# Kernel tuning notes

Measured on AMD Instinct MI355X. Metric: run time of the kernel, lower is better.

## Reference

```python
import jax, jax.numpy as jnp
import numpy as np

LN_EPS = 1e-12
NEG_INF = -1e9


def setup_inputs() -> dict:
    key = jax.random.key(0)
    ks = jax.random.split(key, 4)
    B, S, H = 8, 2048, 1024
    inputs = jax.random.normal(ks[0], (B, S, H), dtype=jnp.float32)
    masks = jnp.ones((B, S), dtype=jnp.int32)
    scale = 1.0 / np.sqrt(H)
    Wq = jax.random.normal(ks[1], (H, H), dtype=jnp.float32) * scale
    bq = jnp.zeros((H,), dtype=jnp.float32)
    Wk = jax.random.normal(ks[2], (H, H), dtype=jnp.float32) * scale
    bk = jnp.zeros((H,), dtype=jnp.float32)
    ln_gamma = jnp.ones((H,), dtype=jnp.float32)
    ln_beta = jnp.zeros((H,), dtype=jnp.float32)
    return {"inputs": inputs, "masks": masks, "Wq": Wq, "bq": bq,
            "Wk": Wk, "bk": bk, "ln_gamma": ln_gamma, "ln_beta": ln_beta}


def _layernorm(x, gamma, beta):
    mu = jnp.mean(x, axis=-1, keepdims=True)
    var = jnp.mean(jnp.square(x - mu), axis=-1, keepdims=True)
    return (x - mu) * jax.lax.rsqrt(var + LN_EPS) * gamma + beta


def reference(inputs, masks, Wq, bq, Wk, bk, ln_gamma, ln_beta):
    # inputs: [B,S,H]; masks: [B,S] (1 = keep key position)
    H = inputs.shape[-1]
    query = inputs @ Wq + bq                      # [B,S,H]
    key_ = inputs @ Wk + bk                       # [B,S,H]
    scores = jnp.einsum('bqh,bkh->bqk', query, key_) * (1.0 / jnp.sqrt(jnp.float32(H)))
    # logits_mask: invalid key positions get large negative logit
    scores = jnp.where(masks[:, None, :] != 0, scores, NEG_INF)
    probs = jax.nn.softmax(scores, axis=-1)       # [B,S,S]
    context = jnp.einsum('bqk,bkh->bqh', probs, inputs)  # value = raw inputs
    return _layernorm(inputs + context, ln_gamma, ln_beta)
```

## Files before the change

### kernel.cpp

```cpp
#include <hip/hip_runtime.h>
#include <stdint.h>
#include <stddef.h>

typedef _Float16 f16_t;
typedef _Float16 f16x8 __attribute__((ext_vector_type(8)));
typedef _Float16 f16x4 __attribute__((ext_vector_type(4)));
typedef float    f32x4 __attribute__((ext_vector_type(4)));

#define AS_G __attribute__((address_space(1)))
#define AS_L __attribute__((address_space(3)))

__device__ __forceinline__ void gload_lds16(const void* g, void* l) {
  __builtin_amdgcn_global_load_lds((const AS_G uint32_t*)g, (AS_L uint32_t*)l, 16, 0, 0);
}

#define LN_EPS 1e-12f

__global__ __launch_bounds__(256) void cast_f16_kernel(const float* __restrict__ in,
                                                       f16_t* __restrict__ out) {
  int i = blockIdx.x * 256 + threadIdx.x;
  float4 v = ((const float4*)in)[i];
  f16x4 o = {(f16_t)v.x, (f16_t)v.y, (f16_t)v.z, (f16_t)v.w};
  ((f16x4*)out)[i] = o;
}

__global__ __launch_bounds__(256) void xprep_kernel(const float* __restrict__ in,
                                                    f16_t* __restrict__ xb,
                                                    f16_t* __restrict__ xt) {
  __shared__ float tile[32][33];
  int b = blockIdx.z;
  const float* inb = in + (size_t)b * 2048 * 1024;
  f16_t* xbb = xb + (size_t)b * 2048 * 1024;
  f16_t* xtb = xt + (size_t)b * 1024 * 2048;
  int tx = threadIdx.x, ty = threadIdx.y;
  int c0 = blockIdx.x * 32, r0 = blockIdx.y * 32;
#pragma unroll
  for (int i = 0; i < 32; i += 8) {
    float v = inb[(size_t)(r0 + ty + i) * 1024 + (c0 + tx)];
    tile[ty + i][tx] = v;
    xbb[(size_t)(r0 + ty + i) * 1024 + (c0 + tx)] = (f16_t)v;
  }
  __syncthreads();
#pragma unroll
  for (int i = 0; i < 32; i += 8)
    xtb[(size_t)(c0 + ty + i) * 2048 + (r0 + tx)] = (f16_t)tile[tx][ty + i];
}

__global__ __launch_bounds__(256) void wvec_kernel(const float* __restrict__ Wq,
                                                   const float* __restrict__ bq,
                                                   const float* __restrict__ Wk,
                                                   const float* __restrict__ bk,
                                                   float* __restrict__ wqbk,
                                                   float* __restrict__ wkbq,
                                                   float* __restrict__ c0) {
  __shared__ float red[4];
  int bid = blockIdx.x, tid = threadIdx.x;
  const float* rowp; const float* vecp; float* outp;
  if (bid < 1024)      { rowp = Wq + (size_t)bid * 1024; vecp = bk; outp = wqbk + bid; }
  else if (bid < 2048) { rowp = Wk + (size_t)(bid - 1024) * 1024; vecp = bq; outp = wkbq + (bid - 1024); }
  else                 { rowp = bq; vecp = bk; outp = c0; }
  float4 a = ((const float4*)rowp)[tid];
  float4 b = ((const float4*)vecp)[tid];
  float s = a.x * b.x + a.y * b.y + a.z * b.z + a.w * b.w;
#pragma unroll
  for (int off = 32; off > 0; off >>= 1) s += __shfl_xor(s, off, 64);
  if ((tid & 63) == 0) red[tid >> 6] = s;
  __syncthreads();
  if (tid == 0) *outp = red[0] + red[1] + red[2] + red[3];
}

__global__ __launch_bounds__(256) void cqck_kernel(const float* __restrict__ X,
                                                   const float* __restrict__ wqbk,
                                                   const float* __restrict__ wkbq,
                                                   float* __restrict__ cq,
                                                   float* __restrict__ ck) {
  __shared__ float r1[4], r2[4];
  int m = blockIdx.x, tid = threadIdx.x;
  float4 x = ((const float4*)(X + (size_t)m * 1024))[tid];
  float4 a = ((const float4*)wqbk)[tid];
  float4 b = ((const float4*)wkbq)[tid];
  float s1 = x.x * a.x + x.y * a.y + x.z * a.z + x.w * a.w;
  float s2 = x.x * b.x + x.y * b.y + x.z * b.z + x.w * b.w;
#pragma unroll
  for (int off = 32; off > 0; off >>= 1) { s1 += __shfl_xor(s1, off, 64); s2 += __shfl_xor(s2, off, 64); }
  if ((tid & 63) == 0) { r1[tid >> 6] = s1; r2[tid >> 6] = s2; }
  __syncthreads();
  if (tid == 0) {
    cq[m] = r1[0] + r1[1] + r1[2] + r1[3];
    ck[m] = r2[0] + r2[1] + r2[2] + r2[3];
  }
}

__global__ __launch_bounds__(256) void gemm_bt_kernel(
    const f16_t* __restrict__ A, const f16_t* __restrict__ Bt, f16_t* __restrict__ C,
    const float* __restrict__ cq, const float* __restrict__ ck, const float* __restrict__ c0p,
    const int* __restrict__ mask, const float* __restrict__ invl, float* __restrict__ lpart,
    int lda, int ldb, int ldc, int K, float scale, int mode,
    size_t sA, size_t sB, size_t sC) {
  __shared__ f16_t As[128 * 64];
  __shared__ f16_t Bs[128 * 64];

  const int tid = threadIdx.x;
  const int lane = tid & 63;
  const int wv = tid >> 6;
  const int m16 = lane & 15;
  const int quad = lane >> 4;
  const int wr = (wv >> 1) * 64;
  const int wc = (wv & 1) * 64;

  const f16_t* Ab = A + blockIdx.z * sA + (size_t)blockIdx.x * 128 * lda;
  const f16_t* Bb = Bt + blockIdx.z * sB + (size_t)blockIdx.y * 128 * ldb;

  const int lr8 = lane >> 3;
  const int ch8 = (lane & 7) ^ lr8;
  const f16_t* gA[4]; const f16_t* gB[4];
  f16_t* lA[4]; f16_t* lB[4];
#pragma unroll
  for (int j = 0; j < 4; ++j) {
    int row = wv * 32 + j * 8 + lr8;
    gA[j] = Ab + (size_t)row * lda + ch8 * 8;
    gB[j] = Bb + (size_t)row * ldb + ch8 * 8;
    lA[j] = &As[(wv * 32 + j * 8) * 64];
    lB[j] = &Bs[(wv * 32 + j * 8) * 64];
  }

  int aoff[4], boff[4], swz[2];
#pragma unroll
  for (int t = 0; t < 4; ++t) {
    aoff[t] = (wr + t * 16 + m16) * 64;
    boff[t] = (wc + t * 16 + m16) * 64;
  }
#pragma unroll
  for (int s = 0; s < 2; ++s)
    swz[s] = (((s << 2) | quad) ^ (m16 & 7)) * 8;

  f32x4 acc[4][4] = {};

  for (int k0 = 0; k0 < K; k0 += 64) {
#pragma unroll
    for (int j = 0; j < 4; ++j) {
      gload_lds16(gA[j] + k0, lA[j]);
      gload_lds16(gB[j] + k0, lB[j]);
    }
    __syncthreads();

#pragma unroll
    for (int s = 0; s < 2; ++s) {
      f16x8 af[4], bfr[4];
#pragma unroll
      for (int t = 0; t < 4; ++t) {
        af[t]  = *(const f16x8*)&As[aoff[t] + swz[s]];
        bfr[t] = *(const f16x8*)&Bs[boff[t] + swz[s]];
      }
#pragma unroll
      for (int rt = 0; rt < 4; ++rt)
#pragma unroll
        for (int ct = 0; ct < 4; ++ct)
          acc[rt][ct] = __builtin_amdgcn_mfma_f32_16x16x32_f16(af[rt], bfr[ct], acc[rt][ct], 0, 0, 0);
    }
    __syncthreads();
  }

  f16_t* Cb = C + blockIdx.z * sC;
  const int row0 = blockIdx.x * 128 + wr + quad * 4;
  const int col0 = blockIdx.y * 128 + wc + m16;
  if (mode == 0) {
#pragma unroll
    for (int ct = 0; ct < 4; ++ct)
#pragma unroll
      for (int rt = 0; rt < 4; ++rt)
#pragma unroll
        for (int r = 0; r < 4; ++r)
          Cb[(size_t)(row0 + rt * 16 + r) * ldc + col0 + ct * 16] = (f16_t)acc[rt][ct][r];
  } else if (mode == 1) {
    const int* mp = mask + blockIdx.z * 2048;
    const size_t rowg0 = blockIdx.z * 2048 + row0;
    const float c0 = *c0p;
    float rsum[4][4];
#pragma unroll
    for (int rt = 0; rt < 4; ++rt)
#pragma unroll
      for (int r = 0; r < 4; ++r) rsum[rt][r] = 0.f;
#pragma unroll
    for (int ct = 0; ct < 4; ++ct) {
      int col = col0 + ct * 16;
      bool keep = (mp[col] != 0);
      float ckv = ck[blockIdx.z * 2048 + col];
#pragma unroll
      for (int rt = 0; rt < 4; ++rt)
#pragma unroll
        for (int r = 0; r < 4; ++r) {
          float cqv = cq[rowg0 + rt * 16 + r];
          float p = keep ? __expf((acc[rt][ct][r] + cqv + ckv + c0) * scale) : 0.f;
          rsum[rt][r] += p;
          Cb[(size_t)(row0 + rt * 16 + r) * ldc + col] = (f16_t)p;
        }
    }
    const int chunk = blockIdx.y * 2 + (wv & 1);
#pragma unroll
    for (int rt = 0; rt < 4; ++rt)
#pragma unroll
      for (int r = 0; r < 4; ++r) {
        float v = rsum[rt][r];
        v += __shfl_xor(v, 1, 16);
        v += __shfl_xor(v, 2, 16);
        v += __shfl_xor(v, 4, 16);
        v += __shfl_xor(v, 8, 16);
        if (m16 == 0) lpart[(rowg0 + rt * 16 + r) * 32 + chunk] = v;
      }
  } else {
    const size_t rowg0 = blockIdx.z * 2048 + row0;
#pragma unroll
    for (int rt = 0; rt < 4; ++rt)
#pragma unroll
      for (int r = 0; r < 4; ++r) {
        float il = invl[rowg0 + rt * 16 + r];
#pragma unroll
        for (int ct = 0; ct < 4; ++ct)
          Cb[(size_t)(row0 + rt * 16 + r) * ldc + col0 + ct * 16] = (f16_t)(acc[rt][ct][r] * il);
      }
  }
}

__global__ __launch_bounds__(256) void lreduce_kernel(const float* __restrict__ lpart,
                                                      float* __restrict__ invl) {
  int m = blockIdx.x * 256 + threadIdx.x;
  const float4* p = (const float4*)(lpart + (size_t)m * 32);
  float s = 0.f;
#pragma unroll
  for (int j = 0; j < 8; ++j) {
    float4 v = p[j];
    s += v.x + v.y + v.z + v.w;
  }
  invl[m] = 1.0f / fmaxf(s, 1e-30f);
}

__global__ __launch_bounds__(256) void ln_kernel(const float* __restrict__ X,
                                                 const f16_t* __restrict__ Ctx,
                                                 const float* __restrict__ gamma,
                                                 const float* __restrict__ beta,
                                                 float* __restrict__ out) {
  __shared__ float r1[4], r2[4];
  const int tid = threadIdx.x;
  const size_t base = (size_t)blockIdx.x * 1024;
  float4 xv = ((const float4*)(X + base))[tid];
  f16x4 cv = ((const f16x4*)(Ctx + base))[tid];
  float v0 = xv.x + (float)cv[0];
  float v1 = xv.y + (float)cv[1];
  float v2 = xv.z + (float)cv[2];
  float v3 = xv.w + (float)cv[3];
  float s1 = v0 + v1 + v2 + v3;
  float s2 = v0 * v0 + v1 * v1 + v2 * v2 + v3 * v3;
#pragma unroll
  for (int off = 32; off > 0; off >>= 1) {
    s1 += __shfl_xor(s1, off, 64);
    s2 += __shfl_xor(s2, off, 64);
  }
  if ((tid & 63) == 0) { r1[tid >> 6] = s1; r2[tid >> 6] = s2; }
  __syncthreads();
  s1 = r1[0] + r1[1] + r1[2] + r1[3];
  s2 = r2[0] + r2[1] + r2[2] + r2[3];
  float mu = s1 * (1.0f / 1024.0f);
  float var = s2 * (1.0f / 1024.0f) - mu * mu;
  float rs = rsqrtf(fmaxf(var, 0.0f) + LN_EPS);
  float4 gv = ((const float4*)gamma)[tid];
  float4 bv = ((const float4*)beta)[tid];
  float4 o;
  o.x = (v0 - mu) * rs * gv.x + bv.x;
  o.y = (v1 - mu) * rs * gv.y + bv.y;
  o.z = (v2 - mu) * rs * gv.z + bv.z;
  o.w = (v3 - mu) * rs * gv.w + bv.w;
  ((float4*)(out + base))[tid] = o;
}

extern "C" void kernel_launch(void* const* d_in, const int* in_sizes, int n_in,
                              void* d_out, int out_size, void* d_ws, size_t ws_size,
                              hipStream_t stream) {
  const float* X     = (const float*)d_in[0];
  const int*   masks = (const int*)d_in[1];
  const float* Wq    = (const float*)d_in[2];
  const float* bq    = (const float*)d_in[3];
  const float* Wk    = (const float*)d_in[4];
  const float* bk    = (const float*)d_in[5];
  const float* gamma = (const float*)d_in[6];
  const float* beta  = (const float*)d_in[7];
  float* out = (float*)d_out;

  if (ws_size < 115343360u) return;
  char* ws = (char*)d_ws;
  f16_t* Xb   = (f16_t*)(ws + 0);
  f16_t* Xt   = (f16_t*)(ws + 33554432);
  f16_t* T    = (f16_t*)(ws + 67108864);
  f16_t* Wqf  = (f16_t*)(ws + 100663296);
  f16_t* Wkf  = (f16_t*)(ws + 102760448);
  f16_t* Wkq  = (f16_t*)(ws + 104857600);
  float* lpart= (float*)(ws + 106954752);
  float* cq   = (float*)(ws + 109051904);
  float* ck   = (float*)(ws + 109117440);
  float* invl = (float*)(ws + 109182976);
  float* wqbk = (float*)(ws + 109248512);
  float* wkbq = (float*)(ws + 109252608);
  float* c0   = (float*)(ws + 109256704);
  f16_t* Ctx  = Xb;
  f16_t* probs = (f16_t*)d_out;

  const size_t SH = 2048u * 1024u;
  const size_t SS = 2048u * 2048u;
  const size_t HS = 1024u * 2048u;

  xprep_kernel<<<dim3(32, 64, 8), dim3(32, 8), 0, stream>>>(X, Xb, Xt);
  cast_f16_kernel<<<1024, 256, 0, stream>>>(Wq, Wqf);
  cast_f16_kernel<<<1024, 256, 0, stream>>>(Wk, Wkf);
  wvec_kernel<<<2049, 256, 0, stream>>>(Wq, bq, Wk, bk, wqbk, wkbq, c0);
  cqck_kernel<<<16384, 256, 0, stream>>>(X, wqbk, wkbq, cq, ck);

  gemm_bt_kernel<<<dim3(8, 8, 1), 256, 0, stream>>>(
      Wkf, Wqf, Wkq, nullptr, nullptr, nullptr, nullptr, nullptr, nullptr,
      1024, 1024, 1024, 1024, 0.f, 0, 0, 0, 0);

  gemm_bt_kernel<<<dim3(128, 8, 1), 256, 0, stream>>>(
      Xb, Wkq, T, nullptr, nullptr, nullptr, nullptr, nullptr, nullptr,
      1024, 1024, 1024, 1024, 0.f, 0, 0, 0, 0);

  gemm_bt_kernel<<<dim3(16, 16, 8), 256, 0, stream>>>(
      T, Xb, probs, cq, ck, c0, masks, nullptr, lpart,
      1024, 1024, 2048, 1024, 0.03125f, 1, SH, SH, SS);

  lreduce_kernel<<<64, 256, 0, stream>>>(lpart, invl);

  gemm_bt_kernel<<<dim3(16, 8, 8), 256, 0, stream>>>(
      probs, Xt, Ctx, nullptr, nullptr, nullptr, nullptr, invl, nullptr,
      2048, 2048, 1024, 2048, 0.f, 2, SS, HS, SH);

  ln_kernel<<<16384, 256, 0, stream>>>(X, Ctx, gamma, beta, out);
}
```

Measured before the change: 483.4 us.

## Double-buffer LDS tiles in GEMM to overlap global loads with MFMA

The GEMM main loop now uses two LDS buffers per operand. The next K tile is issued into one buffer via global_load_lds while MFMAs consume the other, and the loop is unrolled by two K steps. This aims to hide global-memory latency behind compute. It doubles LDS use to 64KB per block, which may lower occupancy, and it assumes K is a multiple of 128.

```diff
diff --git a/kernel.cpp b/kernel.cpp
--- a/kernel.cpp
+++ b/kernel.cpp
@@ -97,8 +97,8 @@
     const int* __restrict__ mask, const float* __restrict__ invl, float* __restrict__ lpart,
     int lda, int ldb, int ldc, int K, float scale, int mode,
     size_t sA, size_t sB, size_t sC) {
-  __shared__ f16_t As[128 * 64];
-  __shared__ f16_t Bs[128 * 64];
+  __shared__ f16_t As[2][128 * 64];
+  __shared__ f16_t Bs[2][128 * 64];
 
   const int tid = threadIdx.x;
   const int lane = tid & 63;
@@ -120,8 +120,8 @@
     int row = wv * 32 + j * 8 + lr8;
     gA[j] = Ab + (size_t)row * lda + ch8 * 8;
     gB[j] = Bb + (size_t)row * ldb + ch8 * 8;
-    lA[j] = &As[(wv * 32 + j * 8) * 64];
-    lB[j] = &Bs[(wv * 32 + j * 8) * 64];
+    lA[j] = &As[0][(wv * 32 + j * 8) * 64];
+    lB[j] = &Bs[0][(wv * 32 + j * 8) * 64];
   }
 
   int aoff[4], boff[4], swz[2];
@@ -136,30 +136,43 @@
 
   f32x4 acc[4][4] = {};
 
-  for (int k0 = 0; k0 < K; k0 += 64) {
-#pragma unroll
-    for (int j = 0; j < 4; ++j) {
-      gload_lds16(gA[j] + k0, lA[j]);
-      gload_lds16(gB[j] + k0, lB[j]);
-    }
+#define STAGE(BUF, KOFF)                                       \
+  _Pragma("unroll")                                            \
+  for (int j = 0; j < 4; ++j) {                                \
+    gload_lds16(gA[j] + (KOFF), lA[j] + (BUF) * (128 * 64));   \
+    gload_lds16(gB[j] + (KOFF), lB[j] + (BUF) * (128 * 64));   \
+  }
+
+#define COMPUTE(BUF)                                                           \
+  _Pragma("unroll")                                                            \
+  for (int s = 0; s < 2; ++s) {                                                \
+    f16x8 af[4], bfr[4];                                                       \
+    _Pragma("unroll")                                                          \
+    for (int t = 0; t < 4; ++t) {                                              \
+      af[t]  = *(const f16x8*)&As[BUF][aoff[t] + swz[s]];                      \
+      bfr[t] = *(const f16x8*)&Bs[BUF][boff[t] + swz[s]];                      \
+    }                                                                          \
+    _Pragma("unroll")                                                          \
+    for (int rt = 0; rt < 4; ++rt)                                             \
+      _Pragma("unroll")                                                        \
+      for (int ct = 0; ct < 4; ++ct)                                           \
+        acc[rt][ct] = __builtin_amdgcn_mfma_f32_16x16x32_f16(af[rt], bfr[ct],  \
+                                                             acc[rt][ct], 0, 0, 0); \
+  }
+
+  STAGE(0, 0);
+  __syncthreads();
+
+  for (int k0 = 0; k0 < K; k0 += 128) {
+    STAGE(1, k0 + 64);
+    COMPUTE(0);
     __syncthreads();
-
-#pragma unroll
-    for (int s = 0; s < 2; ++s) {
-      f16x8 af[4], bfr[4];
-#pragma unroll
-      for (int t = 0; t < 4; ++t) {
-        af[t]  = *(const f16x8*)&As[aoff[t] + swz[s]];
-        bfr[t] = *(const f16x8*)&Bs[boff[t] + swz[s]];
-      }
-#pragma unroll
-      for (int rt = 0; rt < 4; ++rt)
-#pragma unroll
-        for (int ct = 0; ct < 4; ++ct)
-          acc[rt][ct] = __builtin_amdgcn_mfma_f32_16x16x32_f16(af[rt], bfr[ct], acc[rt][ct], 0, 0, 0);
-    }
+    if (k0 + 128 < K) STAGE(0, k0 + 128);
+    COMPUTE(1);
     __syncthreads();
   }
+#undef STAGE
+#undef COMPUTE
 
   f16_t* Cb = C + blockIdx.z * sC;
   const int row0 = blockIdx.x * 128 + wr + quad * 4;
```

Result: faster. 471.6 us (-2.4%).
